# Performance work log

Hardware: AMD Instinct MI355X
Metric: run time of the kernel (lower is better)

## Reference

```python
import jax, jax.numpy as jnp
import numpy as np

B, N_PER = 1048576, 32
MAX_COUNT = 5  # counts >= 5 lumped into the '>4' bucket (severity 3)


def setup_inputs() -> dict:
    key = jax.random.key(0)
    k1, k2, k3 = jax.random.split(key, 3)
    x1 = jax.random.uniform(k1, (B, N_PER), dtype=jnp.float32)
    x2 = jax.random.uniform(k2, (B, N_PER), dtype=jnp.float32)
    x3 = jax.random.uniform(k3, (B, N_PER), dtype=jnp.float32)
    return {"x1": x1, "x2": x2, "x3": x3}


def _count_distribution(p):
    # p: [B, N] independent fact probabilities.
    # Poisson-binomial DP over facts with count capped at MAX_COUNT (absorbing).
    b = p.shape[0]
    init = jnp.zeros((b, MAX_COUNT + 1), p.dtype).at[:, 0].set(1.0)

    def step(c, pi):
        pi = pi[:, None]                              # [B,1]
        shifted = jnp.pad(c[:, :-1], ((0, 0), (1, 0)))  # count+1
        new = c * (1.0 - pi) + shifted * pi
        # absorbing top bucket: staying in >=MAX_COUNT regardless of pi
        new = new.at[:, -1].add(c[:, -1] * pi[:, 0])
        return new, None

    counts, _ = jax.lax.scan(step, init, p.T)  # scan over facts axis
    return counts  # [B, MAX_COUNT+1]


def reference(x1, x2, x3):
    p = jnp.concatenate([x1, x2, x3], axis=1)  # [B, 96]
    c = _count_distribution(p)
    # severity(0): n==0; severity(1): 1<=n<=2; severity(2): 3<=n<=4;
    # severity(3): n>4; severity(4): never derivable -> 0
    sev = jnp.stack(
        [c[:, 0], c[:, 1] + c[:, 2], c[:, 3] + c[:, 4], c[:, 5],
         jnp.zeros_like(c[:, 0])],
        axis=1,
    )
    return sev  # [B, 5]
```

## Files before the change

### kernel.cpp

```cpp
#include <hip/hip_runtime.h>


#define THREADS 256

__global__ __launch_bounds__(THREADS, 6) void hemorrhage_kernel(
    const float* __restrict__ x1,
    const float* __restrict__ x2,
    const float* __restrict__ x3,
    float* __restrict__ out)
{
    const int t = threadIdx.x;
    const int m = t & 7;
    const int row = blockIdx.x * (THREADS / 8) + (t >> 3);
    const size_t base = (size_t)row * 32 + (size_t)m * 4;

    const float4 p1 = *(const float4*)(x1 + base);
    const float4 p2 = *(const float4*)(x2 + base);
    const float4 p3 = *(const float4*)(x3 + base);

    float a0 = 1.0f, a1 = 0.0f, a2 = 0.0f, a3 = 0.0f, a4 = 0.0f, a5 = 0.0f;

#define STEP(P)                          \
    do {                                 \
        const float p_ = (P);            \
        const float q_ = 1.0f - p_;      \
        a5 = fmaf(a4, p_, a5);           \
        a4 = fmaf(a4, q_, a3 * p_);      \
        a3 = fmaf(a3, q_, a2 * p_);      \
        a2 = fmaf(a2, q_, a1 * p_);      \
        a1 = fmaf(a1, q_, a0 * p_);      \
        a0 = a0 * q_;                    \
    } while (0)

    STEP(p1.x); STEP(p1.y); STEP(p1.z); STEP(p1.w);
    STEP(p2.x); STEP(p2.y); STEP(p2.z); STEP(p2.w);
    STEP(p3.x); STEP(p3.y); STEP(p3.z); STEP(p3.w);
#undef STEP

#pragma unroll
    for (int d = 1; d < 8; d <<= 1) {
        const float b0 = __shfl_xor(a0, d);
        const float b1 = __shfl_xor(a1, d);
        const float b2 = __shfl_xor(a2, d);
        const float b3 = __shfl_xor(a3, d);
        const float b4 = __shfl_xor(a4, d);
        const float b5 = __shfl_xor(a5, d);

        float n0 = a0 * b0;
        float n1 = a0 * b1;
        n1 = fmaf(a1, b0, n1);
        float n2 = a0 * b2;
        n2 = fmaf(a1, b1, n2);
        n2 = fmaf(a2, b0, n2);
        float n3 = a0 * b3;
        n3 = fmaf(a1, b2, n3);
        n3 = fmaf(a2, b1, n3);
        n3 = fmaf(a3, b0, n3);
        float n4 = a0 * b4;
        n4 = fmaf(a1, b3, n4);
        n4 = fmaf(a2, b2, n4);
        n4 = fmaf(a3, b1, n4);
        n4 = fmaf(a4, b0, n4);
        const float n5 = 1.0f - (((n0 + n1) + (n2 + n3)) + n4);

        a0 = n0; a1 = n1; a2 = n2; a3 = n3; a4 = n4; a5 = n5;
    }

    if (m < 5) {
        float v;
        switch (m) {
            case 0: v = a0; break;
            case 1: v = a1 + a2; break;
            case 2: v = a3 + a4; break;
            case 3: v = a5; break;
            default: v = 0.0f; break;
        }
        out[(size_t)row * 5 + m] = v;
    }
}

extern "C" void kernel_launch(void* const* d_in, const int* in_sizes, int n_in,
                              void* d_out, int out_size, void* d_ws, size_t ws_size,
                              hipStream_t stream) {
    const float* x1 = (const float*)d_in[0];
    const float* x2 = (const float*)d_in[1];
    const float* x3 = (const float*)d_in[2];
    float* out = (float*)d_out;

    const int rows = in_sizes[0] / 32;
    const int blocks = rows / (THREADS / 8);
    hemorrhage_kernel<<<blocks, THREADS, 0, stream>>>(x1, x2, x3, out);
}
```

Baseline: 346.6 us.

## Use four lanes per row with wider loads and drop explicit top bucket

Each row is now handled by four lanes instead of eight. Each lane loads two float4s from every input and runs 24 DP steps before a two-round shuffle combine, down from three rounds. The absorbing top-bucket accumulator is removed everywhere; the top severity is recovered at the end as one minus the other buckets. All five outputs per row are written by four lanes. This cuts shuffle and convolution work and puts more loads in flight per thread, at the cost of a longer serial DP chain and lower occupancy bounds.

```diff
diff --git a/kernel.cpp b/kernel.cpp
--- a/kernel.cpp
+++ b/kernel.cpp
@@ -2,49 +2,58 @@
 
 
 #define THREADS 256
+#define LANES_PER_ROW 4
+#define ROWS_PER_BLOCK (THREADS / LANES_PER_ROW)
 
-__global__ __launch_bounds__(THREADS, 6) void hemorrhage_kernel(
+__global__ __launch_bounds__(THREADS, 4) void hemorrhage_kernel(
     const float* __restrict__ x1,
     const float* __restrict__ x2,
     const float* __restrict__ x3,
     float* __restrict__ out)
 {
     const int t = threadIdx.x;
-    const int m = t & 7;
-    const int row = blockIdx.x * (THREADS / 8) + (t >> 3);
-    const size_t base = (size_t)row * 32 + (size_t)m * 4;
+    const int q4 = t & 3;
+    const int row = blockIdx.x * ROWS_PER_BLOCK + (t >> 2);
+    const size_t fbase = (size_t)row * 32 + (size_t)q4 * 8;
 
-    const float4 p1 = *(const float4*)(x1 + base);
-    const float4 p2 = *(const float4*)(x2 + base);
-    const float4 p3 = *(const float4*)(x3 + base);
+    const float4* s1 = (const float4*)(x1 + fbase);
+    const float4* s2 = (const float4*)(x2 + fbase);
+    const float4* s3 = (const float4*)(x3 + fbase);
+    const float4 v0 = s1[0];
+    const float4 v1 = s1[1];
+    const float4 v2 = s2[0];
+    const float4 v3 = s2[1];
+    const float4 v4 = s3[0];
+    const float4 v5 = s3[1];
 
-    float a0 = 1.0f, a1 = 0.0f, a2 = 0.0f, a3 = 0.0f, a4 = 0.0f, a5 = 0.0f;
+    float a0 = 1.0f, a1 = 0.0f, a2 = 0.0f, a3 = 0.0f, a4 = 0.0f;
 
 #define STEP(P)                          \
     do {                                 \
         const float p_ = (P);            \
         const float q_ = 1.0f - p_;      \
-        a5 = fmaf(a4, p_, a5);           \
         a4 = fmaf(a4, q_, a3 * p_);      \
         a3 = fmaf(a3, q_, a2 * p_);      \
-        a2 = fmaf(a2, q_, a1 * p_);      \
+        a2 = fmaf(a2, q_, a1 * p_);     \
         a1 = fmaf(a1, q_, a0 * p_);      \
         a0 = a0 * q_;                    \
     } while (0)
 
-    STEP(p1.x); STEP(p1.y); STEP(p1.z); STEP(p1.w);
-    STEP(p2.x); STEP(p2.y); STEP(p2.z); STEP(p2.w);
-    STEP(p3.x); STEP(p3.y); STEP(p3.z); STEP(p3.w);
+    STEP(v0.x); STEP(v0.y); STEP(v0.z); STEP(v0.w);
+    STEP(v1.x); STEP(v1.y); STEP(v1.z); STEP(v1.w);
+    STEP(v2.x); STEP(v2.y); STEP(v2.z); STEP(v2.w);
+    STEP(v3.x); STEP(v3.y); STEP(v3.z); STEP(v3.w);
+    STEP(v4.x); STEP(v4.y); STEP(v4.z); STEP(v4.w);
+    STEP(v5.x); STEP(v5.y); STEP(v5.z); STEP(v5.w);
 #undef STEP
 
 #pragma unroll
-    for (int d = 1; d < 8; d <<= 1) {
+    for (int d = 1; d < LANES_PER_ROW; d <<= 1) {
         const float b0 = __shfl_xor(a0, d);
         const float b1 = __shfl_xor(a1, d);
         const float b2 = __shfl_xor(a2, d);
         const float b3 = __shfl_xor(a3, d);
         const float b4 = __shfl_xor(a4, d);
-        const float b5 = __shfl_xor(a5, d);
 
         float n0 = a0 * b0;
         float n1 = a0 * b1;
@@ -61,22 +70,23 @@
         n4 = fmaf(a2, b2, n4);
         n4 = fmaf(a3, b1, n4);
         n4 = fmaf(a4, b0, n4);
-        const float n5 = 1.0f - (((n0 + n1) + (n2 + n3)) + n4);
 
-        a0 = n0; a1 = n1; a2 = n2; a3 = n3; a4 = n4; a5 = n5;
+        a0 = n0; a1 = n1; a2 = n2; a3 = n3; a4 = n4;
     }
 
-    if (m < 5) {
-        float v;
-        switch (m) {
-            case 0: v = a0; break;
-            case 1: v = a1 + a2; break;
-            case 2: v = a3 + a4; break;
-            case 3: v = a5; break;
-            default: v = 0.0f; break;
-        }
-        out[(size_t)row * 5 + m] = v;
-    }
+    const float sev0 = a0;
+    const float sev1 = a1 + a2;
+    const float sev2 = a3 + a4;
+    const float sev3 = 1.0f - (sev0 + sev1 + sev2);
+
+    float vstore = sev3;
+    if (q4 == 0) vstore = sev0;
+    else if (q4 == 1) vstore = sev1;
+    else if (q4 == 2) vstore = sev2;
+
+    float* orow = out + (size_t)row * 5;
+    orow[q4] = vstore;
+    if (q4 == 0) orow[4] = 0.0f;
 }
 
 extern "C" void kernel_launch(void* const* d_in, const int* in_sizes, int n_in,
@@ -88,6 +98,6 @@
     float* out = (float*)d_out;
 
     const int rows = in_sizes[0] / 32;
-    const int blocks = rows / (THREADS / 8);
+    const int blocks = rows / ROWS_PER_BLOCK;
     hemorrhage_kernel<<<blocks, THREADS, 0, stream>>>(x1, x2, x3, out);
 }
```

New measurement: 349.8 us. No clear change (+0.9%).
